# Optimization experiments

Hardware: AMD Instinct MI355X
Metric: run time of the kernel (lower is better)

The kernel has to match this reference:

```python
import jax, jax.numpy as jnp
import numpy as np

N = 50000
E = 1600000
F_IN = 256
HEADS = 4
HID = 32
C = 16
NEG_SLOPE = 0.2


def _add_self_loops(edge_index, n):
    loop = jnp.arange(n, dtype=edge_index.dtype)
    return jnp.concatenate([edge_index, jnp.stack([loop, loop])], axis=1)


def gat_conv(x, edge_index, W, att_src, att_dst, bias, heads, n):
    # PyG GATConv (concat=True, add_self_loops=True, inference: no dropout)
    ei = _add_self_loops(edge_index, n)
    src, dst = ei[0], ei[1]
    d = W.shape[1] // heads
    xw = (x @ W).reshape(n, heads, d)                      # [N,H,D]
    a_src = jnp.sum(xw * att_src, axis=-1)                 # [N,H]
    a_dst = jnp.sum(xw * att_dst, axis=-1)                 # [N,H]
    e = jax.nn.leaky_relu(a_src[src] + a_dst[dst], NEG_SLOPE)  # [E',H]
    # segment softmax over destination neighborhoods
    m = jax.ops.segment_max(e, dst, num_segments=n)        # [N,H]
    ex = jnp.exp(e - m[dst])
    denom = jax.ops.segment_sum(ex, dst, num_segments=n)   # [N,H]
    alpha = ex / denom[dst]                                # [E',H]
    msg = xw[src] * alpha[:, :, None]                      # [E',H,D]
    out = jax.ops.segment_sum(msg, dst, num_segments=n)    # [N,H,D]
    return out.reshape(n, heads * d) + bias


def setup_inputs() -> dict:
    key = jax.random.key(0)
    ks = jax.random.split(key, 10)
    g = lambda k, shape, fan: jax.random.normal(k, shape, jnp.float32) * (1.0 / np.sqrt(fan))
    x = jax.random.normal(ks[0], (N, F_IN), jnp.float32)
    edge_index = jax.random.randint(ks[1], (2, E), 0, N, dtype=jnp.int64)
    return {
        "x": x,
        "edge_index": edge_index,
        "W1": g(ks[2], (F_IN, HEADS * HID), F_IN),
        "att_src1": g(ks[3], (HEADS, HID), HID),
        "att_dst1": g(ks[4], (HEADS, HID), HID),
        "b1": jnp.zeros((HEADS * HID,), jnp.float32),
        "W2": g(ks[5], (HEADS * HID, C), HEADS * HID),
        "att_src2": g(ks[6], (1, C), C),
        "att_dst2": g(ks[7], (1, C), C),
        "b2": jnp.zeros((C,), jnp.float32),
    }


def reference(x, edge_index, W1, att_src1, att_dst1, b1, W2, att_src2, att_dst2, b2):
    h = gat_conv(x, edge_index, W1, att_src1, att_dst1, b1, HEADS, N)
    h = jax.nn.relu(h)
    # dropout: identity at inference (training=False)
    out = gat_conv(h, edge_index, W2, att_src2, att_dst2, b2, 1, N)
    return jax.nn.log_softmax(out, axis=1)
```

## Files before the change

### kernel.cpp

```cpp
#include <hip/hip_runtime.h>
#include <hip/hip_bf16.h>

typedef __hip_bfloat16 bf16;
typedef long long i64;
typedef unsigned long long u64;
typedef __attribute__((ext_vector_type(8))) short short8;
typedef __attribute__((ext_vector_type(4))) float floatx4;

#define NN    50000
#define EE    1600000
#define E2    1650000
#define FIN   256
#define HD    128
#define NH    4
#define NC    16
#define SLOPE 0.2f
#define KB    256
#define DPB   196
#define CAPB  8960
#define CAP   8960
#define CH2   2048
#define GBC   782
#define EBC   806

#define KS_S  2312

#define OF_FLAGS 0
#define OF_BCUR  16
#define OF_BBASE 272
#define OF_RP    544
#define OF_W1T   50548
#define OF_BIN   66932
#define OF_CSR   4654452
#define OF_XQ    6304452
#define OF_SC    7904452
#define OF_AS1   8004452
#define OF_AD1   8204452
#define OF_HW2   8404452
#define OF_AS2   9204452
#define OF_AD2   9254452

__device__ __forceinline__ float b2f(bf16 v) { return __bfloat162float(v); }
__device__ __forceinline__ float us2f(unsigned short u) {
    return __uint_as_float(((unsigned)u) << 16);
}
__device__ __forceinline__ unsigned short f2us(float f) {
    unsigned u = __float_as_uint(f);
    return (unsigned short)((u + 0x7fffu + ((u >> 16) & 1u)) >> 16);
}
__device__ __forceinline__ float lrelu(float v) { return v > 0.f ? v : SLOPE * v; }
__device__ __forceinline__ float ub2f(unsigned u, int sh) {
    return (float)((u >> sh) & 0xffu);
}
__device__ __forceinline__ int fwi(int node, int ch) {
    return node * 132 + (ch >> 5) * 33 + (ch & 31);
}

template <bool F32>
__device__ __forceinline__ float ldin(const void* p, int i) {
    if (F32) return ((const float*)p)[i];
    return b2f(((const bf16*)p)[i]);
}
template <bool F32>
__device__ __forceinline__ float4 ldin4(const void* p, int i) {
    if (F32) return *(const float4*)((const float*)p + i);
    ushort4 u = *(const ushort4*)((const unsigned short*)p + i);
    float4 r;
    r.x = us2f(u.x); r.y = us2f(u.y); r.z = us2f(u.z); r.w = us2f(u.w);
    return r;
}

__device__ __forceinline__ void edge_sd(const void* ei, int f64, int e, int& s, int& d) {
    if (e >= EE) { s = e - EE; d = s; return; }
    if (f64) {
        s = (int)((const i64*)ei)[e];
        d = (int)((const i64*)ei)[EE + e];
    } else {
        s = ((const int*)ei)[e];
        d = ((const int*)ei)[EE + e];
    }
    s = min(max(s, 0), NN - 1);
    d = min(max(d, 0), NN - 1);
}

__global__ void detect(const void* x, const void* ei, int* flags, int* bcur) {
    __shared__ int cnt[2];
    int t = threadIdx.x;
    if (t < KB) bcur[t] = t * CAPB;
    if (t == 0) { cnt[0] = 0; cnt[1] = 0; }
    __syncthreads();
    const unsigned short* xb = (const unsigned short*)x;
    int c0 = 0;
    for (int i = t; i < 4096; i += 256) {
        float v = __uint_as_float(((unsigned)xb[2 * i]) << 16);
        if (!(fabsf(v) < 1e6f)) c0++;
    }
    const i64* e64 = (const i64*)ei;
    int c1 = 0;
    for (int i = t; i < 1024; i += 256) {
        i64 v = e64[i];
        if (v >= 0 && v < NN) c1++;
    }
    atomicAdd(&cnt[0], c0);
    atomicAdd(&cnt[1], c1);
    __syncthreads();
    if (t == 0) {
        flags[0] = (cnt[0] > 400) ? 1 : 0;
        flags[1] = (cnt[1] >= 1000) ? 1 : 0;
    }
}

template <bool F32>
__global__ void trW(const void* __restrict__ W1, const int* __restrict__ flags,
                    unsigned short* __restrict__ w1t) {
    if (flags[0] != (F32 ? 1 : 0)) return;
    int t = blockIdx.x * 256 + threadIdx.x;
    int k = t >> 5, n4 = (t & 31) * 4;
    float4 v = ldin4<F32>(W1, k * HD + n4);
    int ks = k >> 5, kk = k & 31;
    w1t[((ks * HD + n4 + 0) * 32) + kk] = f2us(v.x);
    w1t[((ks * HD + n4 + 1) * 32) + kk] = f2us(v.y);
    w1t[((ks * HD + n4 + 2) * 32) + kk] = f2us(v.z);
    w1t[((ks * HD + n4 + 3) * 32) + kk] = f2us(v.w);
}

template <bool F32>
__global__ __launch_bounds__(256) void gsFuse(
    const void* __restrict__ x, const unsigned short* __restrict__ w1t,
    const void* __restrict__ as1, const void* __restrict__ ad1,
    const void* __restrict__ ei, const int* __restrict__ flags,
    signed char* __restrict__ xq, float* __restrict__ sc2,
    float* __restrict__ asrc, float* __restrict__ adst,
    int* __restrict__ bcur, u64* __restrict__ bin) {
    __shared__ unsigned short af[8 * KS_S];
    __shared__ float scl[128];
    __shared__ int hh[KB], res[KB];
    int t = threadIdx.x;

    if (blockIdx.x >= GBC) {
        int base = (blockIdx.x - GBC) * CH2 + t * 8;
        if (t < KB) hh[t] = 0;
        __syncthreads();
        int f64 = flags[1];
        int sv[8], dv[8], rk[8];
        int n_ = 0;
        if (!f64 && base + 8 <= EE) {
            const int* es = (const int*)ei;
            int4 a = *(const int4*)&es[base];
            int4 b = *(const int4*)&es[base + 4];
            int4 c = *(const int4*)&es[EE + base];
            int4 g = *(const int4*)&es[EE + base + 4];
            sv[0] = a.x; sv[1] = a.y; sv[2] = a.z; sv[3] = a.w;
            sv[4] = b.x; sv[5] = b.y; sv[6] = b.z; sv[7] = b.w;
            dv[0] = c.x; dv[1] = c.y; dv[2] = c.z; dv[3] = c.w;
            dv[4] = g.x; dv[5] = g.y; dv[6] = g.z; dv[7] = g.w;
#pragma unroll
            for (int i = 0; i < 8; i++) {
                sv[i] = min(max(sv[i], 0), NN - 1);
                dv[i] = min(max(dv[i], 0), NN - 1);
            }
            n_ = 8;
        } else {
            for (int i = 0; i < 8; i++) {
                int e = base + i;
                if (e < E2) {
                    int s, d; edge_sd(ei, f64, e, s, d);
                    sv[n_] = s; dv[n_] = d; n_++;
                }
            }
        }
#pragma unroll 8
        for (int i = 0; i < n_; i++) rk[i] = atomicAdd(&hh[dv[i] / DPB], 1);
        __syncthreads();
        if (t < KB) res[t] = hh[t] ? atomicAdd(&bcur[t], hh[t]) : 0;
        __syncthreads();
#pragma unroll 8
        for (int i = 0; i < n_; i++) {
            int b = dv[i] / DPB;
            int pos = res[b] + rk[i];
            pos = min(pos, (b + 1) * CAPB - 1);
            bin[pos] = (((u64)(unsigned)dv[i]) << 32) | (unsigned)sv[i];
        }
        return;
    }

    if (flags[0] != (F32 ? 1 : 0)) return;
    int m0 = blockIdx.x * 64;
#pragma unroll
    for (int i = 0; i < 16; i++) {
        int slot = i * 256 + t;
        int mi = slot >> 6, k4 = (slot & 63) * 4;
        float4 v = make_float4(0.f, 0.f, 0.f, 0.f);
        if (m0 + mi < NN) v = ldin4<F32>(x, (m0 + mi) * FIN + k4);
        ushort4 o;
        o.x = f2us(v.x); o.y = f2us(v.y); o.z = f2us(v.z); o.w = f2us(v.w);
        *(ushort4*)&af[(k4 >> 5) * KS_S + mi * 36 + (k4 & 31)] = o;
    }
    __syncthreads();
    int w = t >> 6, lane = t & 63;
    int col = lane & 15, q = lane >> 4;
    floatx4 acc[4][2];
#pragma unroll
    for (int mt = 0; mt < 4; mt++)
#pragma unroll
        for (int u = 0; u < 2; u++) { acc[mt][u].x = 0.f; acc[mt][u].y = 0.f; acc[mt][u].z = 0.f; acc[mt][u].w = 0.f; }
#pragma unroll
    for (int ks = 0; ks < 8; ks++) {
        short8 bf0 = *(const short8*)&w1t[(ks * HD + w * 32 + col) * 32 + q * 8];
        short8 bf1 = *(const short8*)&w1t[(ks * HD + w * 32 + 16 + col) * 32 + q * 8];
#pragma unroll
        for (int mt = 0; mt < 4; mt++) {
            short8 afr = *(const short8*)&af[ks * KS_S + (mt * 16 + col) * 36 + q * 8];
            acc[mt][0] = __builtin_amdgcn_mfma_f32_16x16x32_bf16(afr, bf0, acc[mt][0], 0, 0, 0);
            acc[mt][1] = __builtin_amdgcn_mfma_f32_16x16x32_bf16(afr, bf1, acc[mt][1], 0, 0, 0);
        }
    }
    __syncthreads();
    float* fw = (float*)af;
#pragma unroll
    for (int mt = 0; mt < 4; mt++)
#pragma unroll
        for (int u = 0; u < 2; u++)
#pragma unroll
            for (int r = 0; r < 4; r++) {
                int node = mt * 16 + q * 4 + r;
                fw[fwi(node, w * 32 + u * 16 + col)] = acc[mt][u][r];
            }
    __syncthreads();
    int node = t >> 2, part = t & 3;
    {
        float amax = 0.f;
#pragma unroll
        for (int c = 0; c < 32; c++) amax = fmaxf(amax, fabsf(fw[fwi(node, part * 32 + c)]));
        amax = fmaxf(amax, __shfl_xor(amax, 1));
        if ((part & 1) == 0) {
            scl[node * 2 + (part >> 1)] = (amax > 0.f) ? 127.f / amax : 0.f;
            if (m0 + node < NN) sc2[(m0 + node) * 2 + (part >> 1)] = amax * (1.f / 127.f);
        }
    }
    __syncthreads();
    if (m0 + node < NN) {
        float inv = scl[node * 2 + (part >> 1)];
        unsigned dw[8];
#pragma unroll
        for (int g = 0; g < 8; g++) {
            unsigned pk = 0;
#pragma unroll
            for (int j = 0; j < 4; j++) {
                float v = fw[fwi(node, part * 32 + g * 4 + j)];
                int qi = (int)rintf(v * inv);
                qi = min(127, max(-127, qi));
                pk |= ((unsigned)((qi + 128) & 255)) << (8 * j);
            }
            dw[g] = pk;
        }
        *(uint4*)&xq[(m0 + node) * HD + part * 32]      = make_uint4(dw[0], dw[1], dw[2], dw[3]);
        *(uint4*)&xq[(m0 + node) * HD + part * 32 + 16] = make_uint4(dw[4], dw[5], dw[6], dw[7]);
        float s = 0.f, dd = 0.f;
#pragma unroll
        for (int c = 0; c < 32; c++) {
            float xv = fw[fwi(node, part * 32 + c)];
            s  += xv * ldin<F32>(as1, part * 32 + c);
            dd += xv * ldin<F32>(ad1, part * 32 + c);
        }
        asrc[(m0 + node) * NH + part] = s;
        adst[(m0 + node) * NH + part] = dd;
    }
}

__global__ __launch_bounds__(256) void csrB(const int* __restrict__ bcur,
                                            const u64* __restrict__ bin,
                                            int* __restrict__ rp, int* __restrict__ csr) {
    __shared__ int cnt[512];
    __shared__ int cur[DPB];
    __shared__ int buf[CAP];
    __shared__ int sc[KB];
    int b = blockIdx.x, t = threadIdx.x;
    sc[t] = min(bcur[t] - t * CAPB, CAPB);
    __syncthreads();
    for (int off = 1; off < KB; off <<= 1) {
        int u = (t >= off) ? sc[t - off] : 0;
        __syncthreads();
        sc[t] += u;
        __syncthreads();
    }
    int base = b ? sc[b - 1] : 0;
    int size = sc[b] - base;
    if (b == KB - 1 && t == 0) rp[NN] = sc[KB - 1];
    int d0 = b * DPB;
    int nd = min(DPB, NN - d0);
    int src0 = b * CAPB;
    cnt[t] = 0; cnt[t + 256] = 0;
    __syncthreads();
    for (int i = t; i < size; i += 256) {
        int d = (int)(bin[src0 + i] >> 32);
        atomicAdd(&cnt[d - d0], 1);
    }
    __syncthreads();
    int a0 = cnt[2 * t], a1 = cnt[2 * t + 1];
    int ps = a0 + a1;
    buf[t] = ps;
    __syncthreads();
    for (int off = 1; off < 256; off <<= 1) {
        int u = (t >= off) ? buf[t - off] : 0;
        __syncthreads();
        buf[t] += u;
        __syncthreads();
    }
    int ex = buf[t] - ps;
    __syncthreads();
    cnt[2 * t] = ex;
    cnt[2 * t + 1] = ex + a0;
    __syncthreads();
    for (int i = t; i < nd; i += 256) {
        rp[d0 + i] = base + cnt[i];
        cur[i] = cnt[i];
    }
    __syncthreads();
    if (size <= CAP) {
        for (int i = t; i < size; i += 256) {
            u64 p = bin[src0 + i];
            int pos = atomicAdd(&cur[(int)(p >> 32) - d0], 1);
            buf[pos] = (int)(unsigned)p;
        }
        __syncthreads();
        for (int i = t; i < size; i += 256) csr[base + i] = buf[i];
    } else {
        for (int i = t; i < size; i += 256) {
            u64 p = bin[src0 + i];
            int pos = base + atomicAdd(&cur[(int)(p >> 32) - d0], 1);
            csr[pos] = (int)(unsigned)p;
        }
    }
}

template <bool F32>
__global__ __launch_bounds__(128) void node1(
    const int* __restrict__ rp, const int* __restrict__ cs,
    const float* __restrict__ asrc, const float* __restrict__ adst,
    const signed char* __restrict__ xq, const float* __restrict__ sc2,
    const void* __restrict__ b1, const void* __restrict__ W2,
    const void* __restrict__ as2, const void* __restrict__ ad2,
    const int* __restrict__ flags, float* __restrict__ hw2,
    float* __restrict__ asrc2, float* __restrict__ adst2) {
    if (flags[0] != (F32 ? 1 : 0)) return;
    int d = blockIdx.x, t = threadIdx.x;
    int beg = rp[d], end = rp[d + 1];
    int deg = end - beg;
    __shared__ float sw[64][4];
    __shared__ int   ss[64];
    __shared__ float red[2][HD];
    __shared__ float wv[2][4];
    __shared__ float hs[HD];
    __shared__ float l2[32];
    int hw_ = t & 3;
    float adw = adst[d * NH + hw_];
    int cg = t & 15, eo = t >> 4, head = cg >> 2;
    float acc[8];
#pragma unroll
    for (int j = 0; j < 8; j++) acc[j] = 0.f;
    float wacc = 0.f, wss = 0.f;
    const unsigned* xqu = (const unsigned*)xq;
    int sl = t >> 2;
    int m = min(deg, 64);
    int nIt = (m + 7) >> 3;
    int ec0 = beg + sl, ec1 = beg + sl + 32;
    int s0 = cs[min(ec0, E2 - 1)];
    int s1 = cs[min(ec1, E2 - 1)];
    int sg[8];
#pragma unroll
    for (int k = 0; k < 8; k++)
        if (k < nIt) sg[k] = cs[min(beg + eo + 8 * k, E2 - 1)];
    float a0 = asrc[s0 * NH + hw_];
    float a1 = asrc[s1 * NH + hw_];
    float q0 = sc2[s0 * 2 + (hw_ >> 1)];
    float q1 = sc2[s1 * 2 + (hw_ >> 1)];
    uint2 uv[8];
#pragma unroll
    for (int k = 0; k < 8; k++)
        if (k < nIt) uv[k] = *(const uint2*)&xqu[sg[k] * 32 + cg * 2];
    float w0 = 0.f, c0 = 0.f, w1 = 0.f, c1 = 0.f;
    if (ec0 < end) { w0 = __expf(fminf(lrelu(a0 + adw), 80.f)); c0 = w0 * q0; }
    if (ec1 < end) { w1 = __expf(fminf(lrelu(a1 + adw), 80.f)); c1 = w1 * q1; }
    sw[sl][hw_] = c0;
    sw[sl + 32][hw_] = c1;
    wacc = w0 + w1;
    __syncthreads();
#pragma unroll
    for (int k = 0; k < 8; k++)
        if (k < nIt) {
            float we = sw[eo + 8 * k][head];
            uint2 u = uv[k];
            acc[0] += we * ub2f(u.x, 0);
            acc[1] += we * ub2f(u.x, 8);
            acc[2] += we * ub2f(u.x, 16);
            acc[3] += we * ub2f(u.x, 24);
            acc[4] += we * ub2f(u.y, 0);
            acc[5] += we * ub2f(u.y, 8);
            acc[6] += we * ub2f(u.y, 16);
            acc[7] += we * ub2f(u.y, 24);
            wss += we;
        }
    for (int chb = beg + 64; chb < end; chb += 32) {
        __syncthreads();
        int ec = chb + sl;
        float w = 0.f, wsc = 0.f;
        int s = 0;
        if (ec < end) {
            s = cs[ec];
            w = __expf(fminf(lrelu(asrc[s * NH + hw_] + adw), 80.f));
            wsc = w * sc2[s * 2 + (hw_ >> 1)];
        }
        sw[sl][hw_] = wsc;
        if (hw_ == 0) ss[sl] = s;
        wacc += w;
        __syncthreads();
        int mm = min(32, end - chb);
        for (int e = eo; e < mm; e += 8) {
            float we = sw[e][head];
            int s2 = ss[e];
            uint2 u = *(const uint2*)&xqu[s2 * 32 + cg * 2];
            acc[0] += we * ub2f(u.x, 0);
            acc[1] += we * ub2f(u.x, 8);
            acc[2] += we * ub2f(u.x, 16);
            acc[3] += we * ub2f(u.x, 24);
            acc[4] += we * ub2f(u.y, 0);
            acc[5] += we * ub2f(u.y, 8);
            acc[6] += we * ub2f(u.y, 16);
            acc[7] += we * ub2f(u.y, 24);
            wss += we;
        }
    }
#pragma unroll
    for (int j = 0; j < 8; j++) acc[j] -= 128.f * wss;
    wacc += __shfl_xor(wacc, 4);
    wacc += __shfl_xor(wacc, 8);
    wacc += __shfl_xor(wacc, 16);
    wacc += __shfl_xor(wacc, 32);
    int wid = t >> 6, lane = t & 63;
    if (lane < 4) wv[wid][lane] = wacc;
#pragma unroll
    for (int j = 0; j < 8; j++) {
        acc[j] += __shfl_xor(acc[j], 16);
        acc[j] += __shfl_xor(acc[j], 32);
    }
    if (lane < 16) {
#pragma unroll
        for (int j = 0; j < 8; j++) red[wid][lane * 8 + j] = acc[j];
    }
    __syncthreads();
    float tot = red[0][t] + red[1][t];
    float wt  = wv[0][t >> 5] + wv[1][t >> 5];
    hs[t] = fmaxf(tot / wt + ldin<F32>(b1, t), 0.f);
    __syncthreads();
    int j = t & 15, g = t >> 4;
    float p = 0.f;
#pragma unroll
    for (int k = 0; k < 16; k++) p += hs[g * 16 + k] * ldin<F32>(W2, (g * 16 + k) * NC + j);
    p += __shfl_xor(p, 16);
    p += __shfl_xor(p, 32);
    if ((t & 63) < 16) l2[(t >> 6) * 16 + j] = p;
    __syncthreads();
    if (t < 16) {
        float hw = l2[t] + l2[16 + t];
        hw2[d * NC + t] = hw;
        float a2s = hw * ldin<F32>(as2, t);
        float a2d = hw * ldin<F32>(ad2, t);
#pragma unroll
        for (int off = 8; off; off >>= 1) {
            a2s += __shfl_xor(a2s, off, 16);
            a2d += __shfl_xor(a2d, off, 16);
        }
        if (t == 0) { asrc2[d] = a2s; adst2[d] = a2d; }
    }
}

template <bool F32>
__global__ __launch_bounds__(256) void node2(
    const int* __restrict__ rp, const int* __restrict__ cs,
    const float* __restrict__ asrc2, const float* __restrict__ adst2,
    const float* __restrict__ hw2, const void* __restrict__ b2,
    const int* __restrict__ flags, void* __restrict__ out) {
    if (flags[0] != (F32 ? 1 : 0)) return;
    int t = threadIdx.x, wid = t >> 6, lane = t & 63;
    int d = blockIdx.x * 4 + wid;
    if (d >= NN) return;
    int beg = rp[d], end = rp[d + 1];
    float ad = adst2[d];
    int q = lane & 3, eo = lane >> 2;
    float4 acc = make_float4(0.f, 0.f, 0.f, 0.f);
    float wtot = 0.f;
    for (int chb = beg; chb < end; chb += 64) {
        int ec = chb + lane;
        int s = 0;
        bool val = ec < end;
        if (val) s = cs[ec];
        int mm = min(64, end - chb);
        int nk = (mm + 15) >> 4;
        float4 v[4];
        int s2a[4];
#pragma unroll
        for (int k = 0; k < 4; k++)
            if (k < nk) s2a[k] = __shfl(s, eo + k * 16);
#pragma unroll
        for (int k = 0; k < 4; k++)
            if (k < nk) v[k] = *(const float4*)&hw2[s2a[k] * NC + q * 4];
        float w = 0.f;
        if (val) w = __expf(fminf(lrelu(asrc2[s] + ad), 80.f));
        float ws = w;
        ws += __shfl_xor(ws, 1);
        ws += __shfl_xor(ws, 2);
        ws += __shfl_xor(ws, 4);
        ws += __shfl_xor(ws, 8);
        ws += __shfl_xor(ws, 16);
        ws += __shfl_xor(ws, 32);
        wtot += ws;
#pragma unroll
        for (int k = 0; k < 4; k++)
            if (k < nk) {
                float we = __shfl(w, eo + k * 16);
                acc.x += we * v[k].x; acc.y += we * v[k].y;
                acc.z += we * v[k].z; acc.w += we * v[k].w;
            }
    }
#pragma unroll
    for (int off = 4; off < 64; off <<= 1) {
        acc.x += __shfl_xor(acc.x, off);
        acc.y += __shfl_xor(acc.y, off);
        acc.z += __shfl_xor(acc.z, off);
        acc.w += __shfl_xor(acc.w, off);
    }
    float rw = 1.f / wtot;
    float v0 = acc.x * rw + ldin<F32>(b2, q * 4 + 0);
    float v1 = acc.y * rw + ldin<F32>(b2, q * 4 + 1);
    float v2 = acc.z * rw + ldin<F32>(b2, q * 4 + 2);
    float v3 = acc.w * rw + ldin<F32>(b2, q * 4 + 3);
    float mx = fmaxf(fmaxf(v0, v1), fmaxf(v2, v3));
    mx = fmaxf(mx, __shfl_xor(mx, 1));
    mx = fmaxf(mx, __shfl_xor(mx, 2));
    float es = __expf(v0 - mx) + __expf(v1 - mx) + __expf(v2 - mx) + __expf(v3 - mx);
    es += __shfl_xor(es, 1);
    es += __shfl_xor(es, 2);
    float lse = mx + __logf(es);
    if (lane < 4) {
        if (F32) {
            *(float4*)&((float*)out)[d * NC + q * 4] =
                make_float4(v0 - lse, v1 - lse, v2 - lse, v3 - lse);
        } else {
            bf16* o = (bf16*)out + d * NC + q * 4;
            o[0] = __float2bfloat16(v0 - lse); o[1] = __float2bfloat16(v1 - lse);
            o[2] = __float2bfloat16(v2 - lse); o[3] = __float2bfloat16(v3 - lse);
        }
    }
}

extern "C" void kernel_launch(void* const* d_in, const int* in_sizes, int n_in,
                              void* d_out, int out_size, void* d_ws, size_t ws_size,
                              hipStream_t stream) {
    const void* x   = d_in[0];
    const void* ei  = d_in[1];
    const void* W1  = d_in[2];
    const void* as1 = d_in[3];
    const void* ad1 = d_in[4];
    const void* b1  = d_in[5];
    const void* W2  = d_in[6];
    const void* as2 = d_in[7];
    const void* ad2 = d_in[8];
    const void* b2v = d_in[9];

    float* ws = (float*)d_ws;
    int* flags = (int*)(ws + OF_FLAGS);
    int* bcur  = (int*)(ws + OF_BCUR);
    int* rp    = (int*)(ws + OF_RP);
    unsigned short* w1t = (unsigned short*)(ws + OF_W1T);
    u64* bin   = (u64*)(ws + OF_BIN);
    int* csr   = (int*)(ws + OF_CSR);
    signed char* xq = (signed char*)(ws + OF_XQ);
    float* sc2   = ws + OF_SC;
    float* asrc1 = ws + OF_AS1;
    float* adst1 = ws + OF_AD1;
    float* hw2   = ws + OF_HW2;
    float* asrc2 = ws + OF_AS2;
    float* adst2 = ws + OF_AD2;

    detect<<<1, 256, 0, stream>>>(x, ei, flags, bcur);
    trW<true><<<32, 256, 0, stream>>>(W1, flags, w1t);
    gsFuse<true><<<GBC + EBC, 256, 0, stream>>>(x, w1t, as1, ad1, ei, flags, xq, sc2,
                                                asrc1, adst1, bcur, bin);
    csrB<<<KB, 256, 0, stream>>>(bcur, bin, rp, csr);
    node1<true><<<NN, 128, 0, stream>>>(rp, csr, asrc1, adst1, xq, sc2, b1, W2, as2, ad2,
                                        flags, hw2, asrc2, adst2);
    node2<true><<<(NN + 3) / 4, 256, 0, stream>>>(rp, csr, asrc2, adst2, hw2, b2v, flags,
                                                  d_out);
}
```

Baseline: 270.9 us.

## Double CSR bucket count, merge prep kernels, vectorize int64 edge loads

```diff
diff --git a/kernel.cpp b/kernel.cpp
--- a/kernel.cpp
+++ b/kernel.cpp
@@ -6,6 +6,7 @@
 typedef unsigned long long u64;
 typedef __attribute__((ext_vector_type(8))) short short8;
 typedef __attribute__((ext_vector_type(4))) float floatx4;
+typedef __attribute__((ext_vector_type(2))) long long ll2;
 
 #define NN    50000
 #define EE    1600000
@@ -15,10 +16,10 @@
 #define NH    4
 #define NC    16
 #define SLOPE 0.2f
-#define KB    256
-#define DPB   196
-#define CAPB  8960
-#define CAP   8960
+#define KB    512
+#define DPB   98
+#define CAPB  4992
+#define CAP   4992
 #define CH2   2048
 #define GBC   782
 #define EBC   806
@@ -27,18 +28,17 @@
 
 #define OF_FLAGS 0
 #define OF_BCUR  16
-#define OF_BBASE 272
 #define OF_RP    544
 #define OF_W1T   50548
 #define OF_BIN   66932
-#define OF_CSR   4654452
-#define OF_XQ    6304452
-#define OF_SC    7904452
-#define OF_AS1   8004452
-#define OF_AD1   8204452
-#define OF_HW2   8404452
-#define OF_AS2   9204452
-#define OF_AD2   9254452
+#define OF_CSR   5178740
+#define OF_XQ    6828740
+#define OF_SC    8428740
+#define OF_AS1   8528740
+#define OF_AD1   8728740
+#define OF_HW2   8928740
+#define OF_AS2   9728740
+#define OF_AD2   9778740
 
 __device__ __forceinline__ float b2f(bf16 v) { return __bfloat162float(v); }
 __device__ __forceinline__ float us2f(unsigned short u) {
@@ -83,40 +83,53 @@
     d = min(max(d, 0), NN - 1);
 }
 
-__global__ void detect(const void* x, const void* ei, int* flags, int* bcur) {
-    __shared__ int cnt[2];
+__global__ __launch_bounds__(256) void prep(const void* __restrict__ x,
+                                            const void* __restrict__ ei,
+                                            const void* __restrict__ W1,
+                                            int* __restrict__ flags, int* __restrict__ bcur,
+                                            unsigned short* __restrict__ w1t) {
     int t = threadIdx.x;
-    if (t < KB) bcur[t] = t * CAPB;
-    if (t == 0) { cnt[0] = 0; cnt[1] = 0; }
-    __syncthreads();
     const unsigned short* xb = (const unsigned short*)x;
+    if (blockIdx.x == 32) {
+        __shared__ int cnt[2];
+        if (t == 0) { cnt[0] = 0; cnt[1] = 0; }
+        bcur[t] = t * CAPB;
+        bcur[t + 256] = (t + 256) * CAPB;
+        __syncthreads();
+        int c0 = 0;
+        for (int i = t; i < 4096; i += 256) {
+            float v = __uint_as_float(((unsigned)xb[2 * i]) << 16);
+            if (!(fabsf(v) < 1e6f)) c0++;
+        }
+        const i64* e64 = (const i64*)ei;
+        int c1 = 0;
+        for (int i = t; i < 1024; i += 256) {
+            i64 v = e64[i];
+            if (v >= 0 && v < NN) c1++;
+        }
+        atomicAdd(&cnt[0], c0);
+        atomicAdd(&cnt[1], c1);
+        __syncthreads();
+        if (t == 0) {
+            flags[0] = (cnt[0] > 400) ? 1 : 0;
+            flags[1] = (cnt[1] >= 1000) ? 1 : 0;
+        }
+        return;
+    }
+    __shared__ int c0s;
+    if (t == 0) c0s = 0;
+    __syncthreads();
     int c0 = 0;
     for (int i = t; i < 4096; i += 256) {
         float v = __uint_as_float(((unsigned)xb[2 * i]) << 16);
         if (!(fabsf(v) < 1e6f)) c0++;
     }
-    const i64* e64 = (const i64*)ei;
-    int c1 = 0;
-    for (int i = t; i < 1024; i += 256) {
-        i64 v = e64[i];
-        if (v >= 0 && v < NN) c1++;
-    }
-    atomicAdd(&cnt[0], c0);
-    atomicAdd(&cnt[1], c1);
-    __syncthreads();
-    if (t == 0) {
-        flags[0] = (cnt[0] > 400) ? 1 : 0;
-        flags[1] = (cnt[1] >= 1000) ? 1 : 0;
-    }
-}
-
-template <bool F32>
-__global__ void trW(const void* __restrict__ W1, const int* __restrict__ flags,
-                    unsigned short* __restrict__ w1t) {
-    if (flags[0] != (F32 ? 1 : 0)) return;
-    int t = blockIdx.x * 256 + threadIdx.x;
-    int k = t >> 5, n4 = (t & 31) * 4;
-    float4 v = ldin4<F32>(W1, k * HD + n4);
+    atomicAdd(&c0s, c0);
+    __syncthreads();
+    bool f32 = c0s > 400;
+    int g = blockIdx.x * 256 + t;
+    int k = g >> 5, n4 = (g & 31) * 4;
+    float4 v = f32 ? ldin4<true>(W1, k * HD + n4) : ldin4<false>(W1, k * HD + n4);
     int ks = k >> 5, kk = k & 31;
     w1t[((ks * HD + n4 + 0) * 32) + kk] = f2us(v.x);
     w1t[((ks * HD + n4 + 1) * 32) + kk] = f2us(v.y);
@@ -134,12 +147,13 @@
     int* __restrict__ bcur, u64* __restrict__ bin) {
     __shared__ unsigned short af[8 * KS_S];
     __shared__ float scl[128];
-    __shared__ int hh[KB], res[KB];
     int t = threadIdx.x;
 
     if (blockIdx.x >= GBC) {
+        int* hh  = (int*)af;
+        int* res = (int*)af + KB;
         int base = (blockIdx.x - GBC) * CH2 + t * 8;
-        if (t < KB) hh[t] = 0;
+        hh[t] = 0; hh[t + 256] = 0;
         __syncthreads();
         int f64 = flags[1];
         int sv[8], dv[8], rk[8];
@@ -160,6 +174,21 @@
                 dv[i] = min(max(dv[i], 0), NN - 1);
             }
             n_ = 8;
+        } else if (f64 && base + 8 <= EE) {
+            const i64* e64 = (const i64*)ei;
+#pragma unroll
+            for (int i = 0; i < 4; i++) {
+                ll2 sp = *(const ll2*)&e64[base + 2 * i];
+                ll2 dp = *(const ll2*)&e64[EE + base + 2 * i];
+                sv[2 * i]     = (int)sp[0]; sv[2 * i + 1] = (int)sp[1];
+                dv[2 * i]     = (int)dp[0]; dv[2 * i + 1] = (int)dp[1];
+            }
+#pragma unroll
+            for (int i = 0; i < 8; i++) {
+                sv[i] = min(max(sv[i], 0), NN - 1);
+                dv[i] = min(max(dv[i], 0), NN - 1);
+            }
+            n_ = 8;
         } else {
             for (int i = 0; i < 8; i++) {
                 int e = base + i;
@@ -172,7 +201,8 @@
 #pragma unroll 8
         for (int i = 0; i < n_; i++) rk[i] = atomicAdd(&hh[dv[i] / DPB], 1);
         __syncthreads();
-        if (t < KB) res[t] = hh[t] ? atomicAdd(&bcur[t], hh[t]) : 0;
+        res[t] = hh[t] ? atomicAdd(&bcur[t], hh[t]) : 0;
+        res[t + 256] = hh[t + 256] ? atomicAdd(&bcur[t + 256], hh[t + 256]) : 0;
         __syncthreads();
 #pragma unroll 8
         for (int i = 0; i < n_; i++) {
@@ -274,19 +304,25 @@
     __shared__ int cnt[512];
     __shared__ int cur[DPB];
     __shared__ int buf[CAP];
-    __shared__ int sc[KB];
+    __shared__ int sz[KB];
+    __shared__ int sx[256];
     int b = blockIdx.x, t = threadIdx.x;
-    sc[t] = min(bcur[t] - t * CAPB, CAPB);
-    __syncthreads();
-    for (int off = 1; off < KB; off <<= 1) {
-        int u = (t >= off) ? sc[t - off] : 0;
-        __syncthreads();
-        sc[t] += u;
-        __syncthreads();
-    }
-    int base = b ? sc[b - 1] : 0;
-    int size = sc[b] - base;
-    if (b == KB - 1 && t == 0) rp[NN] = sc[KB - 1];
+    sz[t] = min(bcur[t] - t * CAPB, CAPB);
+    sz[t + 256] = min(bcur[t + 256] - (t + 256) * CAPB, CAPB);
+    __syncthreads();
+    int pair = sz[2 * t] + sz[2 * t + 1];
+    sx[t] = pair;
+    __syncthreads();
+    for (int off = 1; off < 256; off <<= 1) {
+        int u = (t >= off) ? sx[t - off] : 0;
+        __syncthreads();
+        sx[t] += u;
+        __syncthreads();
+    }
+    int hp = b >> 1;
+    int base = (hp ? sx[hp - 1] : 0) + ((b & 1) ? sz[b & ~1] : 0);
+    int size = sz[b];
+    if (b == KB - 1 && t == 0) rp[NN] = sx[255];
     int d0 = b * DPB;
     int nd = min(DPB, NN - d0);
     int src0 = b * CAPB;
@@ -583,8 +619,7 @@
     float* asrc2 = ws + OF_AS2;
     float* adst2 = ws + OF_AD2;
 
-    detect<<<1, 256, 0, stream>>>(x, ei, flags, bcur);
-    trW<true><<<32, 256, 0, stream>>>(W1, flags, w1t);
+    prep<<<33, 256, 0, stream>>>(x, ei, W1, flags, bcur, w1t);
     gsFuse<true><<<GBC + EBC, 256, 0, stream>>>(x, w1t, as1, ad1, ei, flags, xq, sc2,
                                                 asrc1, adst1, bcur, bin);
     csrB<<<KB, 256, 0, stream>>>(bcur, bin, rp, csr);
```

Result: faster. 262.1 us, median of 2 (-3.2%).
